# Optimization experiments

Hardware: AMD Instinct MI355X
Metric: run time of the kernel (lower is better)

Reference implementation:

```python
import jax, jax.numpy as jnp
import numpy as np

GRID_SIZE = 5
SPLINE_ORDER = 3
GRID_LO, GRID_HI = -1.0, 1.0


def _make_grid():
    # extended knot vector: grid_size + 2*spline_order intervals
    h = (GRID_HI - GRID_LO) / GRID_SIZE
    return jnp.arange(-SPLINE_ORDER, GRID_SIZE + SPLINE_ORDER + 1, dtype=jnp.float32) * h + GRID_LO


def _b_splines(x, grid):
    # x: [N, F] -> bases [N, F, GRID_SIZE + SPLINE_ORDER] via Cox-de Boor recursion
    xg = x[..., None]
    bases = ((xg >= grid[:-1]) & (xg < grid[1:])).astype(x.dtype)
    for k in range(1, SPLINE_ORDER + 1):
        left = (xg - grid[: -(k + 1)]) / (grid[k:-1] - grid[: -(k + 1)])
        right = (grid[k + 1:] - xg) / (grid[k + 1:] - grid[1:-k])
        bases = left * bases[..., :-1] + right * bases[..., 1:]
    return bases


def _kan_linear(x, base_w, spline_w, spline_scaler, grid):
    # x: [N, in], base_w: [out, in], spline_w: [out, in, K], spline_scaler: [out, in]
    base_out = jax.nn.relu(x) @ base_w.T
    n = x.shape[0]
    sw = (spline_w * spline_scaler[..., None]).reshape(base_w.shape[0], -1)  # [out, in*K]
    spline_out = _b_splines(x, grid).reshape(n, -1) @ sw.T
    return base_out + spline_out


def _kan_conv(x, base_w, spline_w, spline_scaler, grid, k=5):
    # x: [B, C, H, W] -> KANLinear over unfolded 5x5 patches (stride 1, VALID)
    B, C, H, W = x.shape
    patches = jax.lax.conv_general_dilated_patches(x, (k, k), (1, 1), 'VALID')  # [B, C*k*k, Ho, Wo]
    Ho, Wo = patches.shape[2], patches.shape[3]
    p = patches.transpose(0, 2, 3, 1).reshape(B * Ho * Wo, C * k * k)
    out = _kan_linear(p, base_w, spline_w, spline_scaler, grid)
    return out.reshape(B, Ho, Wo, -1).transpose(0, 3, 1, 2)


def _avgpool2(x):
    B, C, H, W = x.shape
    return x.reshape(B, C, H // 2, 2, W // 2, 2).mean(axis=(3, 5))


def setup_inputs() -> dict:
    key = jax.random.key(0)
    ks = jax.random.split(key, 13)
    s = 0.1
    return {
        'x': jax.random.normal(ks[0], (1024, 1, 28, 28), jnp.float32),
        'c1_base_w': jax.random.normal(ks[1], (6, 25), jnp.float32) * s,
        'c1_spline_w': jax.random.normal(ks[2], (6, 25, 8), jnp.float32) * s,
        'c1_spline_scaler': jax.random.normal(ks[3], (6, 25), jnp.float32) * s,
        'c2_base_w': jax.random.normal(ks[4], (16, 150), jnp.float32) * s,
        'c2_spline_w': jax.random.normal(ks[5], (16, 150, 8), jnp.float32) * s,
        'c2_spline_scaler': jax.random.normal(ks[6], (16, 150), jnp.float32) * s,
        'fc1_w': jax.random.normal(ks[7], (120, 256), jnp.float32) * s,
        'fc1_b': jax.random.normal(ks[8], (120,), jnp.float32) * s,
        'fc2_w': jax.random.normal(ks[9], (84, 120), jnp.float32) * s,
        'fc2_b': jax.random.normal(ks[10], (84,), jnp.float32) * s,
        'fc3_w': jax.random.normal(ks[11], (62, 84), jnp.float32) * s,
        'fc3_b': jax.random.normal(ks[12], (62,), jnp.float32) * s,
    }


def reference(x, c1_base_w, c1_spline_w, c1_spline_scaler,
              c2_base_w, c2_spline_w, c2_spline_scaler,
              fc1_w, fc1_b, fc2_w, fc2_b, fc3_w, fc3_b):
    grid = _make_grid()
    h = _kan_conv(x, c1_base_w, c1_spline_w, c1_spline_scaler, grid)   # [B,6,24,24]
    h = _avgpool2(h)                                                    # [B,6,12,12]
    h = _kan_conv(h, c2_base_w, c2_spline_w, c2_spline_scaler, grid)   # [B,16,8,8]
    h = _avgpool2(h)                                                    # [B,16,4,4]
    h = h.reshape(h.shape[0], -1)                                       # [B,256]
    h = jax.nn.relu(h @ fc1_w.T + fc1_b)
    h = jax.nn.relu(h @ fc2_w.T + fc2_b)
    return h @ fc3_w.T + fc3_b                                          # [B,62]
```

## Files before the change

### kernel.cpp

```cpp
#include <hip/hip_runtime.h>


typedef _Float16 f16;
typedef f16 f16x8 __attribute__((ext_vector_type(8)));
typedef float f32x4 __attribute__((ext_vector_type(4)));

#define ONE_SIXTH 0.16666666666666666f

__device__ __forceinline__ void spline9(float v, float* __restrict__ f) {
    float u  = 2.5f * v + 5.5f;
    bool valid = (u >= 0.0f) && (u < 11.0f);
    float fi = floorf(u);
    int   i  = (int)fi;
    float w  = u - fi;
    float omw = 1.0f - w;
    float w2 = w * w, w3 = w2 * w;
    float c0 = omw * omw * omw * ONE_SIXTH;
    float c1 = (3.0f * w3 - 6.0f * w2 + 4.0f) * ONE_SIXTH;
    float c2 = (-3.0f * w3 + 3.0f * w2 + 3.0f * w + 1.0f) * ONE_SIXTH;
    float c3 = w3 * ONE_SIXTH;
    int j0 = i - 3;
#pragma unroll
    for (int j = 0; j < 8; ++j) {
        int d = j - j0;
        float val = (d == 0) ? c0 : (d == 1) ? c1 : (d == 2) ? c2 : (d == 3) ? c3 : 0.0f;
        f[j] = valid ? val : 0.0f;
    }
    f[8] = fmaxf(v, 0.0f);
}

__device__ __forceinline__ void spline_chunks(float v, uint4& u0, uint4& u1) {
    float f[9];
    spline9(v, f);
    union { f16 h[8]; uint4 u; } a, b;
#pragma unroll
    for (int j = 0; j < 8; ++j) a.h[j] = (f16)f[j];
    b.u.x = 0u; b.u.y = 0u; b.u.z = 0u; b.u.w = 0u;
    b.h[0] = (f16)f[8];
    u0 = a.u; u1 = b.u;
}

__global__ __launch_bounds__(256) void k_prep(
    const float* __restrict__ c1_bw, const float* __restrict__ c1_sw,
    const float* __restrict__ c1_sc,
    const float* __restrict__ c2_bw, const float* __restrict__ c2_sw,
    const float* __restrict__ c2_sc,
    f16* __restrict__ W1g, f16* __restrict__ W2g)
{
    int t = blockIdx.x * 256 + threadIdx.x;
    if (t < 9216) {
        int tap = t >> 8, r = t & 255;
        int o = r >> 4, k = r & 15;
        float val = 0.0f;
        if (o < 6 && k < 9) {
            int ey = tap / 6, ex = tap - 6 * ey;
            float s = 0.0f;
            for (int a = 0; a < 2; ++a) {
                for (int b = 0; b < 2; ++b) {
                    int dy = ey - a, dx = ex - b;
                    if (dy >= 0 && dy < 5 && dx >= 0 && dx < 5) {
                        int idx = o * 25 + dy * 5 + dx;
                        s += (k == 8) ? c1_bw[idx] : c1_sw[idx * 8 + k] * c1_sc[idx];
                    }
                }
            }
            val = 0.25f * s;
        }
        W1g[t] = (f16)val;
    }
    if (t < 55296) {
        int c = t / 9216, r = t - c * 9216;
        int tap = r >> 8, rr = r & 255;
        int o = rr >> 4, k = rr & 15;
        float val = 0.0f;
        if (k < 9) {
            int ey = tap / 6, ex = tap - 6 * ey;
            float s = 0.0f;
            for (int a = 0; a < 2; ++a) {
                for (int b = 0; b < 2; ++b) {
                    int dy = ey - a, dx = ex - b;
                    if (dy >= 0 && dy < 5 && dx >= 0 && dx < 5) {
                        int idx = o * 150 + c * 25 + dy * 5 + dx;
                        s += (k == 8) ? c2_bw[idx] : c2_sw[idx * 8 + k] * c2_sc[idx];
                    }
                }
            }
            val = 0.25f * s;
        }
        W2g[t] = (f16)val;
    }
}

__global__ __launch_bounds__(192, 3) void k_conv12(
    const float* __restrict__ x, const f16* __restrict__ W1g,
    const f16* __restrict__ W2g, float* __restrict__ h2)
{
    __shared__ uint4  feat[2016];
    __shared__ float  h1l[864];
    __shared__ float4 rbuf[2][64];

    const int img = blockIdx.x;
    const int tid = threadIdx.x;
    const int lane = tid & 63, wv = tid >> 6;
    const int ln15 = lane & 15, g = lane >> 4;
    const int gh = g & 1, gt = g >> 1;

    {
        const int r0 = 8 * wv;
        float xv[6];
#pragma unroll
        for (int p = 0; p < 6; ++p) {
            int e = lane + p * 64;
            int ee = e < 336 ? e : 335;
            int row = ee / 28, col = ee - row * 28;
            xv[p] = x[img * 784 + (r0 + row) * 28 + col];
        }
#pragma unroll
        for (int p = 0; p < 6; ++p) {
            int e = lane + p * 64;
            if (e < 336) {
                uint4 u0, u1;
                spline_chunks(xv[p], u0, u1);
                int ch = wv * 672 + e * 2;
                int q = (ch >> 3) & 7;
                feat[ch ^ q] = u0;
                feat[(ch + 1) ^ q] = u1;
            }
        }
    }

    {
        int ebase[3];
#pragma unroll
        for (int t = 0; t < 3; ++t) {
            int p = (wv * 3 + t) * 16 + ln15;
            int py = p / 12, px = p - py * 12;
            int row_local = 2 * py - 8 * wv;
            ebase[t] = row_local * 28 + 2 * px;
        }
        const f16* bbase = W1g + (gt * 16 + ln15) * 16 + gh * 8;
        f16x8 wreg[4];
#pragma unroll
        for (int i = 0; i < 4; ++i)
            wreg[i] = *(const f16x8*)(bbase + i * 512);

        f32x4 acc[3] = {{0,0,0,0},{0,0,0,0},{0,0,0,0}};

#pragma unroll
        for (int kc = 0; kc < 18; ++kc) {
            f16x8 bcur = wreg[kc & 3];
            wreg[kc & 3] = *(const f16x8*)(bbase + (kc + 4) * 512);
            int tap = kc * 2 + gt;
            int ey = (tap * 171) >> 10, ex = tap - ey * 6;
            int eoff = ey * 28 + ex;
#pragma unroll
            for (int t = 0; t < 3; ++t) {
                int ch = wv * 672 + (ebase[t] + eoff) * 2 + gh;
                ch ^= (ch >> 3) & 7;
                f16x8 afrag = *(const f16x8*)(&feat[ch]);
                acc[t] = __builtin_amdgcn_mfma_f32_16x16x32_f16(afrag, bcur, acc[t], 0, 0, 0);
            }
        }
        if (ln15 < 6) {
#pragma unroll
            for (int t = 0; t < 3; ++t) {
                int p0 = (wv * 3 + t) * 16 + g * 4;
                *(float4*)&h1l[ln15 * 144 + p0] =
                    make_float4(acc[t][0], acc[t][1], acc[t][2], acc[t][3]);
            }
        }
    }
    __syncthreads();

    {
        float hv[5];
#pragma unroll
        for (int p = 0; p < 5; ++p) {
            int e = lane + p * 64;
            int ee = e < 288 ? e : 287;
            hv[p] = h1l[wv * 288 + ee];
        }
#pragma unroll
        for (int p = 0; p < 5; ++p) {
            int e = lane + p * 64;
            if (e < 288) {
                uint4 u0, u1;
                spline_chunks(hv[p], u0, u1);
                int ch = wv * 576 + e * 2;
                int q = (ch >> 3) & 7;
                feat[ch ^ q] = u0;
                feat[(ch + 1) ^ q] = u1;
            }
        }
    }

    {
        const int py = ln15 >> 2, px = ln15 & 3;
        const int epx = py * 24 + px * 2;
        const int kk0 = wv * 36;
        const f16* bbase = W2g + ((kk0 * 2 + gt) * 16 + ln15) * 16 + gh * 8;
        f16x8 wreg[4];
#pragma unroll
        for (int i = 0; i < 4; ++i)
            wreg[i] = *(const f16x8*)(bbase + i * 512);

        f32x4 accA = {0, 0, 0, 0}, accB = {0, 0, 0, 0};

#pragma unroll
        for (int i = 0; i < 36; ++i) {
            f16x8 bcur = wreg[i & 3];
            wreg[i & 3] = *(const f16x8*)(bbase + (i + 4) * 512);
            int cl = i / 18;
            int tk = i - cl * 18;
            int tap = tk * 2 + gt;
            int ey = (tap * 171) >> 10, ex = tap - ey * 6;
            int elem = cl * 144 + epx + ey * 12 + ex;
            int ch = wv * 576 + elem * 2 + gh;
            ch ^= (ch >> 3) & 7;
            f16x8 afrag = *(const f16x8*)(&feat[ch]);
            if ((i & 1) == 0)
                accA = __builtin_amdgcn_mfma_f32_16x16x32_f16(afrag, bcur, accA, 0, 0, 0);
            else
                accB = __builtin_amdgcn_mfma_f32_16x16x32_f16(afrag, bcur, accB, 0, 0, 0);
        }
        f32x4 acc = accA + accB;

        if (wv) rbuf[wv - 1][lane] = make_float4(acc[0], acc[1], acc[2], acc[3]);
        __syncthreads();
        if (wv == 0) {
            float4 r0 = rbuf[0][lane], r1 = rbuf[1][lane];
            *(float4*)&h2[img * 256 + ln15 * 16 + g * 4] =
                make_float4(acc[0] + r0.x + r1.x, acc[1] + r0.y + r1.y,
                            acc[2] + r0.z + r1.z, acc[3] + r0.w + r1.w);
        }
    }
}

__global__ __launch_bounds__(256) void k_fc(
    const float* __restrict__ h2,
    const float* __restrict__ w1, const float* __restrict__ b1,
    const float* __restrict__ w2, const float* __restrict__ b2,
    const float* __restrict__ w3, const float* __restrict__ b3,
    float* __restrict__ out)
{
    __shared__ float xin[4][260];
    __shared__ float a1[4][120];
    __shared__ float a2[4][84];
    const int tid = threadIdx.x;
    const int r0 = blockIdx.x * 4;

    for (int i = tid; i < 1024; i += 256)
        xin[i >> 8][i & 255] = h2[r0 * 256 + i];
    __syncthreads();

    for (int idx = tid; idx < 480; idx += 256) {
        const int o = idx >> 2, r = idx & 3;
        const float* w = w1 + o * 256;
        float s = 0.0f;
#pragma unroll 8
        for (int k = 0; k < 64; ++k) {
            float4 wv = ((const float4*)w)[k];
            float4 xv = *(const float4*)(&xin[r][k * 4]);
            s += wv.x * xv.x + wv.y * xv.y + wv.z * xv.z + wv.w * xv.w;
        }
        a1[r][o] = fmaxf(s + b1[o], 0.0f);
    }
    __syncthreads();

    for (int idx = tid; idx < 336; idx += 256) {
        const int o = idx >> 2, r = idx & 3;
        const float* w = w2 + o * 120;
        float s = 0.0f;
#pragma unroll
        for (int k = 0; k < 30; ++k) {
            float4 wv = ((const float4*)w)[k];
            float4 xv = *(const float4*)(&a1[r][k * 4]);
            s += wv.x * xv.x + wv.y * xv.y + wv.z * xv.z + wv.w * xv.w;
        }
        a2[r][o] = fmaxf(s + b2[o], 0.0f);
    }
    __syncthreads();

    for (int idx = tid; idx < 248; idx += 256) {
        const int o = idx >> 2, r = idx & 3;
        const float* w = w3 + o * 84;
        float s = 0.0f;
#pragma unroll
        for (int k = 0; k < 21; ++k) {
            float4 wv = ((const float4*)w)[k];
            float4 xv = *(const float4*)(&a2[r][k * 4]);
            s += wv.x * xv.x + wv.y * xv.y + wv.z * xv.z + wv.w * xv.w;
        }
        out[(r0 + r) * 62 + o] = s + b3[o];
    }
}

extern "C" void kernel_launch(void* const* d_in, const int* in_sizes, int n_in,
                              void* d_out, int out_size, void* d_ws, size_t ws_size,
                              hipStream_t stream)
{
    (void)in_sizes; (void)n_in; (void)out_size; (void)ws_size;
    const float* x      = (const float*)d_in[0];
    const float* c1_bw  = (const float*)d_in[1];
    const float* c1_sw  = (const float*)d_in[2];
    const float* c1_sc  = (const float*)d_in[3];
    const float* c2_bw  = (const float*)d_in[4];
    const float* c2_sw  = (const float*)d_in[5];
    const float* c2_sc  = (const float*)d_in[6];
    const float* fc1_w  = (const float*)d_in[7];
    const float* fc1_b  = (const float*)d_in[8];
    const float* fc2_w  = (const float*)d_in[9];
    const float* fc2_b  = (const float*)d_in[10];
    const float* fc3_w  = (const float*)d_in[11];
    const float* fc3_b  = (const float*)d_in[12];
    float* out = (float*)d_out;

    char* wsb = (char*)d_ws;
    f16*   W1g = (f16*)(wsb);
    f16*   W2g = (f16*)(wsb + 18432);
    float* h2  = (float*)(wsb + 139264);

    hipLaunchKernelGGL(k_prep, dim3(256), dim3(256), 0, stream,
                       c1_bw, c1_sw, c1_sc, c2_bw, c2_sw, c2_sc, W1g, W2g);
    hipLaunchKernelGGL(k_conv12, dim3(1024), dim3(192), 0, stream,
                       x, W1g, W2g, h2);
    hipLaunchKernelGGL(k_fc, dim3(256), dim3(256), 0, stream,
                       h2, fc1_w, fc1_b, fc2_w, fc2_b, fc3_w, fc3_b, out);
}
```

Measured before the change: 39.13 us.

## Split conv2 spline and base-weight GEMMs to drop padded K and shrink LDS

Conv2 stage no longer packs the ReLU base term into a padded 16-wide K chunk per tap. It now runs a dense 8-wide spline GEMM plus a separate small base GEMM over ReLU'd activations gathered into LDS, which roughly halves the MFMA work and weight traffic for conv2. Conv1 features are computed once for the full image, and the h1 and reduction buffers alias into the shared feature array. This shrinks LDS so launch bounds can rise to 4 blocks per CU. It costs extra barriers and a more complex gather for the base-term fragments.

```diff
diff --git a/kernel.cpp b/kernel.cpp
--- a/kernel.cpp
+++ b/kernel.cpp
@@ -7,7 +7,7 @@
 
 #define ONE_SIXTH 0.16666666666666666f
 
-__device__ __forceinline__ void spline9(float v, float* __restrict__ f) {
+__device__ __forceinline__ void spline8_vals(float v, float* __restrict__ f) {
     float u  = 2.5f * v + 5.5f;
     bool valid = (u >= 0.0f) && (u < 11.0f);
     float fi = floorf(u);
@@ -26,18 +26,26 @@
         float val = (d == 0) ? c0 : (d == 1) ? c1 : (d == 2) ? c2 : (d == 3) ? c3 : 0.0f;
         f[j] = valid ? val : 0.0f;
     }
-    f[8] = fmaxf(v, 0.0f);
 }
 
 __device__ __forceinline__ void spline_chunks(float v, uint4& u0, uint4& u1) {
-    float f[9];
-    spline9(v, f);
+    float f[8];
+    spline8_vals(v, f);
     union { f16 h[8]; uint4 u; } a, b;
 #pragma unroll
     for (int j = 0; j < 8; ++j) a.h[j] = (f16)f[j];
     b.u.x = 0u; b.u.y = 0u; b.u.z = 0u; b.u.w = 0u;
-    b.h[0] = (f16)f[8];
+    b.h[0] = (f16)fmaxf(v, 0.0f);
     u0 = a.u; u1 = b.u;
+}
+
+__device__ __forceinline__ uint4 spline8_chunk(float v) {
+    float f[8];
+    spline8_vals(v, f);
+    union { f16 h[8]; uint4 u; } a;
+#pragma unroll
+    for (int j = 0; j < 8; ++j) a.h[j] = (f16)f[j];
+    return a.u;
 }
 
 __global__ __launch_bounds__(256) void k_prep(
@@ -45,7 +53,7 @@
     const float* __restrict__ c1_sc,
     const float* __restrict__ c2_bw, const float* __restrict__ c2_sw,
     const float* __restrict__ c2_sc,
-    f16* __restrict__ W1g, f16* __restrict__ W2g)
+    f16* __restrict__ W1g, f16* __restrict__ W2b, f16* __restrict__ W2rT)
 {
     int t = blockIdx.x * 256 + threadIdx.x;
     if (t < 9216) {
@@ -68,66 +76,80 @@
         }
         W1g[t] = (f16)val;
     }
-    if (t < 55296) {
-        int c = t / 9216, r = t - c * 9216;
-        int tap = r >> 8, rr = r & 255;
-        int o = rr >> 4, k = rr & 15;
+    if (t < 27648) {
+        int ct = t >> 7, r = t & 127;
+        int o = r >> 3, k = r & 7;
+        int c = ct / 36, t66 = ct - c * 36;
+        int ey = t66 / 6, ex = t66 - ey * 6;
+        float s = 0.0f;
+        for (int a = 0; a < 2; ++a) {
+            for (int b = 0; b < 2; ++b) {
+                int dy = ey - a, dx = ex - b;
+                if (dy >= 0 && dy < 5 && dx >= 0 && dx < 5) {
+                    int idx = o * 150 + c * 25 + dy * 5 + dx;
+                    s += c2_sw[idx * 8 + k] * c2_sc[idx];
+                }
+            }
+        }
+        W2b[t] = (f16)(0.25f * s);
+    }
+    if (t < 4608) {
+        int o = t / 288, s = t - o * 288;
+        int wq = s / 96, i = s - wq * 96;
         float val = 0.0f;
-        if (k < 9) {
-            int ey = tap / 6, ex = tap - 6 * ey;
-            float s = 0.0f;
+        if (i < 72) {
+            int c = 2 * wq + (i >= 36 ? 1 : 0);
+            int t66 = i - (i >= 36 ? 36 : 0);
+            int ey = t66 / 6, ex = t66 - ey * 6;
+            float acc = 0.0f;
             for (int a = 0; a < 2; ++a) {
                 for (int b = 0; b < 2; ++b) {
                     int dy = ey - a, dx = ex - b;
-                    if (dy >= 0 && dy < 5 && dx >= 0 && dx < 5) {
-                        int idx = o * 150 + c * 25 + dy * 5 + dx;
-                        s += (k == 8) ? c2_bw[idx] : c2_sw[idx * 8 + k] * c2_sc[idx];
-                    }
+                    if (dy >= 0 && dy < 5 && dx >= 0 && dx < 5)
+                        acc += c2_bw[o * 150 + c * 25 + dy * 5 + dx];
                 }
             }
-            val = 0.25f * s;
-        }
-        W2g[t] = (f16)val;
-    }
-}
-
-__global__ __launch_bounds__(192, 3) void k_conv12(
+            val = 0.25f * acc;
+        }
+        W2rT[t] = (f16)val;
+    }
+}
+
+__global__ __launch_bounds__(192, 4) void k_conv12(
     const float* __restrict__ x, const f16* __restrict__ W1g,
-    const f16* __restrict__ W2g, float* __restrict__ h2)
+    const f16* __restrict__ W2b, const f16* __restrict__ W2rT,
+    float* __restrict__ h2)
 {
-    __shared__ uint4  feat[2016];
-    __shared__ float  h1l[864];
-    __shared__ float4 rbuf[2][64];
+    __shared__ uint4 feat[1912];
 
     const int img = blockIdx.x;
     const int tid = threadIdx.x;
     const int lane = tid & 63, wv = tid >> 6;
     const int ln15 = lane & 15, g = lane >> 4;
     const int gh = g & 1, gt = g >> 1;
+    float* h1f = (float*)&feat[1568];
 
     {
-        const int r0 = 8 * wv;
-        float xv[6];
-#pragma unroll
-        for (int p = 0; p < 6; ++p) {
-            int e = lane + p * 64;
-            int ee = e < 336 ? e : 335;
-            int row = ee / 28, col = ee - row * 28;
-            xv[p] = x[img * 784 + (r0 + row) * 28 + col];
-        }
-#pragma unroll
-        for (int p = 0; p < 6; ++p) {
-            int e = lane + p * 64;
-            if (e < 336) {
+        float xv[5];
+#pragma unroll
+        for (int p = 0; p < 5; ++p) {
+            int e = tid + p * 192;
+            xv[p] = x[img * 784 + (e < 784 ? e : 783)];
+        }
+#pragma unroll
+        for (int p = 0; p < 5; ++p) {
+            int e = tid + p * 192;
+            if (e < 784) {
                 uint4 u0, u1;
                 spline_chunks(xv[p], u0, u1);
-                int ch = wv * 672 + e * 2;
+                int ch = e * 2;
                 int q = (ch >> 3) & 7;
                 feat[ch ^ q] = u0;
                 feat[(ch + 1) ^ q] = u1;
             }
         }
     }
+    __syncthreads();
 
     {
         int ebase[3];
@@ -135,8 +157,7 @@
         for (int t = 0; t < 3; ++t) {
             int p = (wv * 3 + t) * 16 + ln15;
             int py = p / 12, px = p - py * 12;
-            int row_local = 2 * py - 8 * wv;
-            ebase[t] = row_local * 28 + 2 * px;
+            ebase[t] = py * 56 + px * 2;
         }
         const f16* bbase = W1g + (gt * 16 + ln15) * 16 + gh * 8;
         f16x8 wreg[4];
@@ -155,7 +176,7 @@
             int eoff = ey * 28 + ex;
 #pragma unroll
             for (int t = 0; t < 3; ++t) {
-                int ch = wv * 672 + (ebase[t] + eoff) * 2 + gh;
+                int ch = (ebase[t] + eoff) * 2 + gh;
                 ch ^= (ch >> 3) & 7;
                 f16x8 afrag = *(const f16x8*)(&feat[ch]);
                 acc[t] = __builtin_amdgcn_mfma_f32_16x16x32_f16(afrag, bcur, acc[t], 0, 0, 0);
@@ -165,7 +186,7 @@
 #pragma unroll
             for (int t = 0; t < 3; ++t) {
                 int p0 = (wv * 3 + t) * 16 + g * 4;
-                *(float4*)&h1l[ln15 * 144 + p0] =
+                *(float4*)&h1f[ln15 * 144 + p0] =
                     make_float4(acc[t][0], acc[t][1], acc[t][2], acc[t][3]);
             }
         }
@@ -173,62 +194,77 @@
     __syncthreads();
 
     {
-        float hv[5];
-#pragma unroll
-        for (int p = 0; p < 5; ++p) {
-            int e = lane + p * 64;
-            int ee = e < 288 ? e : 287;
-            hv[p] = h1l[wv * 288 + ee];
-        }
-#pragma unroll
-        for (int p = 0; p < 5; ++p) {
-            int e = lane + p * 64;
-            if (e < 288) {
-                uint4 u0, u1;
-                spline_chunks(hv[p], u0, u1);
-                int ch = wv * 576 + e * 2;
-                int q = (ch >> 3) & 7;
-                feat[ch ^ q] = u0;
-                feat[(ch + 1) ^ q] = u1;
-            }
-        }
-    }
+        for (int e = tid; e < 864; e += 192) {
+            uint4 u = spline8_chunk(h1f[e]);
+            int ch = e; ch ^= (ch >> 3) & 7;
+            feat[ch] = u;
+        }
+        for (int f = tid; f < 576; f += 192) {
+            int p = f / 36, j = f - (f / 36) * 36;
+            union { f16 h[8]; uint4 u; } r;
+#pragma unroll
+            for (int i = 0; i < 8; ++i) {
+                int s = j * 8 + i;
+                int wq = s / 96, ii = s - wq * 96;
+                float v = 0.0f;
+                if (ii < 72) {
+                    int c = 2 * wq + (ii >= 36 ? 1 : 0);
+                    int t66 = ii - (ii >= 36 ? 36 : 0);
+                    int ey = (t66 * 171) >> 10, ex = t66 - ey * 6;
+                    int epx2 = (p >> 2) * 24 + (p & 3) * 2;
+                    v = fmaxf(h1f[c * 144 + epx2 + ey * 12 + ex], 0.0f);
+                }
+                r.h[i] = (f16)v;
+            }
+            int ch = 864 + p * 36 + j; ch ^= (ch >> 3) & 7;
+            feat[ch] = r.u;
+        }
+    }
+    __syncthreads();
 
     {
-        const int py = ln15 >> 2, px = ln15 & 3;
-        const int epx = py * 24 + px * 2;
-        const int kk0 = wv * 36;
-        const f16* bbase = W2g + ((kk0 * 2 + gt) * 16 + ln15) * 16 + gh * 8;
+        const int epx2 = (ln15 >> 2) * 24 + (ln15 & 3) * 2;
+        const f16* bb = W2b + (72 * wv + g) * 128 + ln15 * 8;
         f16x8 wreg[4];
 #pragma unroll
         for (int i = 0; i < 4; ++i)
-            wreg[i] = *(const f16x8*)(bbase + i * 512);
+            wreg[i] = *(const f16x8*)(bb + i * 512);
+        f16x8 rw[3];
+#pragma unroll
+        for (int r = 0; r < 3; ++r)
+            rw[r] = *(const f16x8*)(W2rT + ln15 * 288 + wv * 96 + r * 32 + g * 8);
 
         f32x4 accA = {0, 0, 0, 0}, accB = {0, 0, 0, 0};
 
 #pragma unroll
-        for (int i = 0; i < 36; ++i) {
-            f16x8 bcur = wreg[i & 3];
-            wreg[i & 3] = *(const f16x8*)(bbase + (i + 4) * 512);
-            int cl = i / 18;
-            int tk = i - cl * 18;
-            int tap = tk * 2 + gt;
-            int ey = (tap * 171) >> 10, ex = tap - ey * 6;
-            int elem = cl * 144 + epx + ey * 12 + ex;
-            int ch = wv * 576 + elem * 2 + gh;
+        for (int q = 0; q < 18; ++q) {
+            f16x8 bcur = wreg[q & 3];
+            wreg[q & 3] = *(const f16x8*)(bb + (q + 4) * 512);
+            int ct = 72 * wv + 4 * q + g;
+            int c = ct / 36, t66 = ct - c * 36;
+            int ey = (t66 * 171) >> 10, ex = t66 - ey * 6;
+            int elem = c * 144 + epx2 + ey * 12 + ex;
+            int ch = elem ^ ((elem >> 3) & 7);
+            f16x8 afrag = *(const f16x8*)(&feat[ch]);
+            if (q & 1)
+                accB = __builtin_amdgcn_mfma_f32_16x16x32_f16(afrag, bcur, accB, 0, 0, 0);
+            else
+                accA = __builtin_amdgcn_mfma_f32_16x16x32_f16(afrag, bcur, accA, 0, 0, 0);
+        }
+#pragma unroll
+        for (int r = 0; r < 3; ++r) {
+            int ch = 864 + ln15 * 36 + wv * 12 + r * 4 + g;
             ch ^= (ch >> 3) & 7;
             f16x8 afrag = *(const f16x8*)(&feat[ch]);
-            if ((i & 1) == 0)
-                accA = __builtin_amdgcn_mfma_f32_16x16x32_f16(afrag, bcur, accA, 0, 0, 0);
-            else
-                accB = __builtin_amdgcn_mfma_f32_16x16x32_f16(afrag, bcur, accB, 0, 0, 0);
+            accA = __builtin_amdgcn_mfma_f32_16x16x32_f16(afrag, rw[r], accA, 0, 0, 0);
         }
         f32x4 acc = accA + accB;
 
-        if (wv) rbuf[wv - 1][lane] = make_float4(acc[0], acc[1], acc[2], acc[3]);
+        float4* rb2 = (float4*)&feat[1784];
+        if (wv) rb2[(wv - 1) * 64 + lane] = make_float4(acc[0], acc[1], acc[2], acc[3]);
         __syncthreads();
         if (wv == 0) {
-            float4 r0 = rbuf[0][lane], r1 = rbuf[1][lane];
+            float4 r0 = rb2[lane], r1 = rb2[64 + lane];
             *(float4*)&h2[img * 256 + ln15 * 16 + g * 4] =
                 make_float4(acc[0] + r0.x + r1.x, acc[1] + r0.y + r1.y,
                             acc[2] + r0.z + r1.z, acc[3] + r0.w + r1.w);
@@ -316,14 +352,15 @@
     float* out = (float*)d_out;
 
     char* wsb = (char*)d_ws;
-    f16*   W1g = (f16*)(wsb);
-    f16*   W2g = (f16*)(wsb + 18432);
-    float* h2  = (float*)(wsb + 139264);
-
-    hipLaunchKernelGGL(k_prep, dim3(256), dim3(256), 0, stream,
-                       c1_bw, c1_sw, c1_sc, c2_bw, c2_sw, c2_sc, W1g, W2g);
+    f16*   W1g  = (f16*)(wsb);
+    f16*   W2b  = (f16*)(wsb + 18432);
+    f16*   W2rT = (f16*)(wsb + 73728);
+    float* h2   = (float*)(wsb + 98304);
+
+    hipLaunchKernelGGL(k_prep, dim3(108), dim3(256), 0, stream,
+                       c1_bw, c1_sw, c1_sc, c2_bw, c2_sw, c2_sc, W1g, W2b, W2rT);
     hipLaunchKernelGGL(k_conv12, dim3(1024), dim3(192), 0, stream,
-                       x, W1g, W2g, h2);
+                       x, W1g, W2b, W2rT, h2);
     hipLaunchKernelGGL(k_fc, dim3(256), dim3(256), 0, stream,
                        h2, fc1_w, fc1_b, fc2_w, fc2_b, fc3_w, fc3_b, out);
 }
```

New measurement: 44.32 us. 13.2% more time.

## Double conv block to six waves with shared feature buffer and split-K conv2

Applied to the files above, without the earlier changes.

The fused conv kernel now runs 384 threads (six waves) per image instead of 192. Layer-1 spline features for the whole image go into one shared buffer rather than per-wave row slabs with duplicated halos, which makes that buffer smaller. The nine conv1 tiles are spread over six waves, two tiles each for three waves and one for the rest. Conv2 is split by input channel across the six waves and reduced through shared memory. This adds barriers and leaves the conv1 work unbalanced across waves, in exchange for more parallelism per image and less redundant spline work.

```diff
diff --git a/kernel.cpp b/kernel.cpp
--- a/kernel.cpp
+++ b/kernel.cpp
@@ -91,13 +91,13 @@
     }
 }
 
-__global__ __launch_bounds__(192, 3) void k_conv12(
+__global__ __launch_bounds__(384, 6) void k_conv12(
     const float* __restrict__ x, const f16* __restrict__ W1g,
     const f16* __restrict__ W2g, float* __restrict__ h2)
 {
-    __shared__ uint4  feat[2016];
+    __shared__ uint4  feat[1728];
     __shared__ float  h1l[864];
-    __shared__ float4 rbuf[2][64];
+    __shared__ float4 rbuf[5][64];
 
     const int img = blockIdx.x;
     const int tid = threadIdx.x;
@@ -106,37 +106,36 @@
     const int gh = g & 1, gt = g >> 1;
 
     {
-        const int r0 = 8 * wv;
-        float xv[6];
-#pragma unroll
-        for (int p = 0; p < 6; ++p) {
-            int e = lane + p * 64;
-            int ee = e < 336 ? e : 335;
-            int row = ee / 28, col = ee - row * 28;
-            xv[p] = x[img * 784 + (r0 + row) * 28 + col];
-        }
-#pragma unroll
-        for (int p = 0; p < 6; ++p) {
-            int e = lane + p * 64;
-            if (e < 336) {
+        float xv[3];
+#pragma unroll
+        for (int p = 0; p < 3; ++p) {
+            int e = tid + p * 384;
+            xv[p] = x[img * 784 + (e < 784 ? e : 783)];
+        }
+#pragma unroll
+        for (int p = 0; p < 3; ++p) {
+            int e = tid + p * 384;
+            if (e < 784) {
                 uint4 u0, u1;
                 spline_chunks(xv[p], u0, u1);
-                int ch = wv * 672 + e * 2;
+                int ch = e * 2;
                 int q = (ch >> 3) & 7;
                 feat[ch ^ q] = u0;
                 feat[(ch + 1) ^ q] = u1;
             }
         }
     }
+    __syncthreads();
 
     {
-        int ebase[3];
-#pragma unroll
-        for (int t = 0; t < 3; ++t) {
-            int p = (wv * 3 + t) * 16 + ln15;
+        const int nt = (wv < 3) ? 2 : 1;
+        int ebase[2];
+#pragma unroll
+        for (int t = 0; t < 2; ++t) {
+            int tile = (t == 0) ? wv : (6 + wv);
+            int p = tile * 16 + ln15;
             int py = p / 12, px = p - py * 12;
-            int row_local = 2 * py - 8 * wv;
-            ebase[t] = row_local * 28 + 2 * px;
+            ebase[t] = py * 56 + px * 2;
         }
         const f16* bbase = W1g + (gt * 16 + ln15) * 16 + gh * 8;
         f16x8 wreg[4];
@@ -144,7 +143,7 @@
         for (int i = 0; i < 4; ++i)
             wreg[i] = *(const f16x8*)(bbase + i * 512);
 
-        f32x4 acc[3] = {{0,0,0,0},{0,0,0,0},{0,0,0,0}};
+        f32x4 acc[2] = {{0,0,0,0},{0,0,0,0}};
 
 #pragma unroll
         for (int kc = 0; kc < 18; ++kc) {
@@ -153,52 +152,55 @@
             int tap = kc * 2 + gt;
             int ey = (tap * 171) >> 10, ex = tap - ey * 6;
             int eoff = ey * 28 + ex;
-#pragma unroll
-            for (int t = 0; t < 3; ++t) {
-                int ch = wv * 672 + (ebase[t] + eoff) * 2 + gh;
+            {
+                int ch = (ebase[0] + eoff) * 2 + gh;
                 ch ^= (ch >> 3) & 7;
                 f16x8 afrag = *(const f16x8*)(&feat[ch]);
-                acc[t] = __builtin_amdgcn_mfma_f32_16x16x32_f16(afrag, bcur, acc[t], 0, 0, 0);
+                acc[0] = __builtin_amdgcn_mfma_f32_16x16x32_f16(afrag, bcur, acc[0], 0, 0, 0);
+            }
+            if (nt == 2) {
+                int ch = (ebase[1] + eoff) * 2 + gh;
+                ch ^= (ch >> 3) & 7;
+                f16x8 afrag = *(const f16x8*)(&feat[ch]);
+                acc[1] = __builtin_amdgcn_mfma_f32_16x16x32_f16(afrag, bcur, acc[1], 0, 0, 0);
             }
         }
         if (ln15 < 6) {
-#pragma unroll
-            for (int t = 0; t < 3; ++t) {
-                int p0 = (wv * 3 + t) * 16 + g * 4;
-                *(float4*)&h1l[ln15 * 144 + p0] =
-                    make_float4(acc[t][0], acc[t][1], acc[t][2], acc[t][3]);
-            }
+            *(float4*)&h1l[ln15 * 144 + wv * 16 + g * 4] =
+                make_float4(acc[0][0], acc[0][1], acc[0][2], acc[0][3]);
+            if (nt == 2)
+                *(float4*)&h1l[ln15 * 144 + (6 + wv) * 16 + g * 4] =
+                    make_float4(acc[1][0], acc[1][1], acc[1][2], acc[1][3]);
         }
     }
     __syncthreads();
 
     {
-        float hv[5];
-#pragma unroll
-        for (int p = 0; p < 5; ++p) {
-            int e = lane + p * 64;
-            int ee = e < 288 ? e : 287;
-            hv[p] = h1l[wv * 288 + ee];
-        }
-#pragma unroll
-        for (int p = 0; p < 5; ++p) {
-            int e = lane + p * 64;
-            if (e < 288) {
+        float hv[3];
+#pragma unroll
+        for (int p = 0; p < 3; ++p) {
+            int e = tid + p * 384;
+            hv[p] = h1l[e < 864 ? e : 863];
+        }
+#pragma unroll
+        for (int p = 0; p < 3; ++p) {
+            int e = tid + p * 384;
+            if (e < 864) {
                 uint4 u0, u1;
                 spline_chunks(hv[p], u0, u1);
-                int ch = wv * 576 + e * 2;
+                int ch = e * 2;
                 int q = (ch >> 3) & 7;
                 feat[ch ^ q] = u0;
                 feat[(ch + 1) ^ q] = u1;
             }
         }
     }
+    __syncthreads();
 
     {
         const int py = ln15 >> 2, px = ln15 & 3;
         const int epx = py * 24 + px * 2;
-        const int kk0 = wv * 36;
-        const f16* bbase = W2g + ((kk0 * 2 + gt) * 16 + ln15) * 16 + gh * 8;
+        const f16* bbase = W2g + (wv * 36 + gt) * 256 + ln15 * 16 + gh * 8;
         f16x8 wreg[4];
 #pragma unroll
         for (int i = 0; i < 4; ++i)
@@ -207,15 +209,13 @@
         f32x4 accA = {0, 0, 0, 0}, accB = {0, 0, 0, 0};
 
 #pragma unroll
-        for (int i = 0; i < 36; ++i) {
+        for (int i = 0; i < 18; ++i) {
             f16x8 bcur = wreg[i & 3];
             wreg[i & 3] = *(const f16x8*)(bbase + (i + 4) * 512);
-            int cl = i / 18;
-            int tk = i - cl * 18;
-            int tap = tk * 2 + gt;
+            int tap = i * 2 + gt;
             int ey = (tap * 171) >> 10, ex = tap - ey * 6;
-            int elem = cl * 144 + epx + ey * 12 + ex;
-            int ch = wv * 576 + elem * 2 + gh;
+            int elem = wv * 144 + epx + ey * 12 + ex;
+            int ch = elem * 2 + gh;
             ch ^= (ch >> 3) & 7;
             f16x8 afrag = *(const f16x8*)(&feat[ch]);
             if ((i & 1) == 0)
@@ -228,10 +228,14 @@
         if (wv) rbuf[wv - 1][lane] = make_float4(acc[0], acc[1], acc[2], acc[3]);
         __syncthreads();
         if (wv == 0) {
-            float4 r0 = rbuf[0][lane], r1 = rbuf[1][lane];
+            float sx = acc[0], sy = acc[1], sz = acc[2], sw = acc[3];
+#pragma unroll
+            for (int r = 0; r < 5; ++r) {
+                float4 rv = rbuf[r][lane];
+                sx += rv.x; sy += rv.y; sz += rv.z; sw += rv.w;
+            }
             *(float4*)&h2[img * 256 + ln15 * 16 + g * 4] =
-                make_float4(acc[0] + r0.x + r1.x, acc[1] + r0.y + r1.y,
-                            acc[2] + r0.z + r1.z, acc[3] + r0.w + r1.w);
+                make_float4(sx, sy, sz, sw);
         }
     }
 }
@@ -322,7 +326,7 @@
 
     hipLaunchKernelGGL(k_prep, dim3(256), dim3(256), 0, stream,
                        c1_bw, c1_sw, c1_sc, c2_bw, c2_sw, c2_sc, W1g, W2g);
-    hipLaunchKernelGGL(k_conv12, dim3(1024), dim3(192), 0, stream,
+    hipLaunchKernelGGL(k_conv12, dim3(1024), dim3(384), 0, stream,
                        x, W1g, W2g, h2);
     hipLaunchKernelGGL(k_fc, dim3(256), dim3(256), 0, stream,
                        h2, fc1_w, fc1_b, fc2_w, fc2_b, fc3_w, fc3_b, out);
```

Result: slower. 40.08 us (+2.4%).
